# Kernel tuning notes

Measured on AMD Instinct MI355X. Metric: run time of the kernel, lower is better.

The kernel has to match this reference:

```python
import jax, jax.numpy as jnp
import numpy as np

N = 50000      # nodes
E = 800000     # edges (avg degree 16)
F_IN = 64      # node_features (== GENConv out, so no input projection)
H = 64         # hidden
EXP = 2 * H    # GENConv MLP expansion dim = 128
D2 = F_IN + H  # dense-block concat dim = SAGEConv in = 128
EPS_MSG = 1e-7 # GENConv message eps
BN_EPS = 1e-5


def setup_inputs() -> dict:
    key = jax.random.key(0)
    ks = jax.random.split(key, 16)
    g = lambda k, shape, fan: jax.random.normal(k, shape, jnp.float32) / np.sqrt(fan)
    return {
        "x": jax.random.normal(ks[0], (N, F_IN), jnp.float32),
        "edge_index": jax.random.randint(ks[1], (2, E), 0, N, jnp.int32),
        # GENConv MLP: Linear(64,128) -> BatchNorm(128) -> ReLU -> Linear(128,64)
        "W1": g(ks[2], (H, EXP), H), "b1": jnp.zeros((EXP,), jnp.float32),
        "gamma": jnp.ones((EXP,), jnp.float32), "beta": jnp.zeros((EXP,), jnp.float32),
        "W2": g(ks[3], (EXP, H), EXP), "b2": jnp.zeros((H,), jnp.float32),
        # SAGEConv project Linear(128,128), lin_l Linear(128,64), lin_r Linear(128,64,bias=False)
        "Wp": g(ks[4], (D2, D2), D2), "bp": jnp.zeros((D2,), jnp.float32),
        "Wl": g(ks[5], (D2, H), D2), "bl": jnp.zeros((H,), jnp.float32),
        "Wr": g(ks[6], (D2, H), D2),
        # fc Linear(64,1)
        "Wf": g(ks[7], (H, 1), H), "bf": jnp.zeros((1,), jnp.float32),
    }


def _forward(x, W1, b1, gamma, beta, W2, b2, Wp, bp, Wl, bl, Wr, Wf, bf, src, dst):
    n = x.shape[0]
    # ---- GENConv(aggr='softmax', t=1.0): msg = relu(x_j) + eps -------------
    msg = jax.nn.relu(x[src]) + EPS_MSG                       # [E, H]
    mmax = jax.ops.segment_max(msg, dst, num_segments=n)      # per-dst, per-feature max
    mmax = jax.lax.stop_gradient(jnp.where(jnp.isfinite(mmax), mmax, 0.0))
    e = jnp.exp(msg - mmax[dst])                              # t = 1.0
    denom = jax.ops.segment_sum(e, dst, num_segments=n)
    numer = jax.ops.segment_sum(e * msg, dst, num_segments=n)
    agg = numer / jnp.where(denom > 0, denom, 1.0)            # softmax aggregation
    out = agg + x                                             # residual with x_dst
    # GENConv MLP (BatchNorm in training mode: batch stats, biased var)
    h = out @ W1 + b1
    mu = h.mean(axis=0)
    var = h.var(axis=0)
    h = (h - mu) * jax.lax.rsqrt(var + BN_EPS) * gamma + beta
    h = jax.nn.relu(h) @ W2 + b2                              # [N, H]
    # ---- DeepGCNLayer block='dense': concat input ---------------------------
    x2 = jnp.concatenate([x, h], axis=-1)                     # [N, F_IN+H]
    x2 = jax.nn.sigmoid(x2)                                   # self.relu = Sigmoid()
    # ---- SAGEConv(project=True, aggr=DeepSetsAggregation()==sum) -----------
    xp = jax.nn.relu(x2 @ Wp + bp)                            # projected source feats
    aggr = jax.ops.segment_sum(xp[src], dst, num_segments=n)  # DeepSets w/o nns = sum
    out2 = aggr @ Wl + bl + x2 @ Wr                           # root uses UNprojected x2
    out2 = jax.nn.sigmoid(out2)
    logits = out2 @ Wf + bf                                   # [N, 1]
    probs = jax.nn.sigmoid(logits)                            # training branch
    return probs, logits


def reference(x, edge_index, W1, b1, gamma, beta, W2, b2, Wp, bp, Wl, bl, Wr, Wf, bf):
    src, dst = edge_index[0], edge_index[1]
    return _forward(x, W1, b1, gamma, beta, W2, b2, Wp, bp, Wl, bl, Wr, Wf, bf, src, dst)
```

## Files before the change

### kernel.cpp

```cpp
#include <hip/hip_runtime.h>

#define F_IN 64
#define HID 64
#define EXPD 128
#define D2 128
#define MAXDEG 64
#define NBW 128
#define NB 391
#define NBINB 98
#define SUBCAP 64
#define EPT 32

typedef __attribute__((ext_vector_type(8))) short bf16x8;
typedef __attribute__((ext_vector_type(4))) float f32x4;

__device__ __forceinline__ float sigmoidf_(float x) {
    return 1.0f / (1.0f + __expf(-x));
}
__device__ __forceinline__ unsigned bf16rne_(float f) {
    unsigned u = __float_as_uint(f);
    return (u + 0x7FFFu + ((u >> 16) & 1u)) >> 16;
}
__device__ __forceinline__ float bf16tof_(unsigned u16) {
    return __uint_as_float(u16 << 16);
}

__global__ __launch_bounds__(256) void k_bin(const int* __restrict__ ei,
                                             int* __restrict__ cnt2,
                                             unsigned* __restrict__ binned2,
                                             const float* __restrict__ x,
                                             unsigned short* __restrict__ x16,
                                             const float* __restrict__ W1,
                                             const float* __restrict__ W2,
                                             const float* __restrict__ Wp,
                                             const float* __restrict__ Wl,
                                             const float* __restrict__ Wr,
                                             short* __restrict__ dst,
                                             float* __restrict__ bnsums,
                                             int nE, int n, int nbinb) {
    int b = blockIdx.x;
    int tid = threadIdx.x;
    if (b < nbinb) {
        __shared__ int hist[NB];
        if (b == 0) bnsums[tid] = 0.f;
        for (int i = tid; i < NB; i += 256) hist[i] = 0;
        __syncthreads();
        unsigned ed[EPT];
        unsigned short rk[EPT];
        int e0 = b * (256 * EPT);
#pragma unroll
        for (int j = 0; j < EPT; ++j) {
            int e = e0 + j * 256 + tid;
            if (e < nE) {
                unsigned s = (unsigned)ei[e];
                unsigned d = (unsigned)ei[nE + e];
                ed[j] = s | (d << 16);
                rk[j] = (unsigned short)atomicAdd(&hist[d >> 7], 1);
            }
        }
        __syncthreads();
        for (int i = tid; i < NB; i += 256) cnt2[b * NB + i] = hist[i];
#pragma unroll
        for (int j = 0; j < EPT; ++j) {
            int e = e0 + j * 256 + tid;
            if (e < nE) {
                int bin = (ed[j] >> 16) >> 7;
                int r = (int)rk[j];
                if (r < SUBCAP)
                    binned2[((size_t)bin * nbinb + b) * SUBCAP + r] = ed[j];
            }
        }
        return;
    }
    b -= nbinb;
    if (b < 192) {
        int e = b * 256 + tid;
        const float* src;
        int K, N, base2;
        if (e < 8192)       { src = W1; K = 64;  N = 128; base2 = 0; }
        else if (e < 16384) { src = W2; K = 128; N = 64;  base2 = 8192; }
        else if (e < 32768) { src = Wp; K = 128; N = 128; base2 = 16384; }
        else if (e < 40960) { src = Wl; K = 128; N = 64;  base2 = 32768; }
        else                { src = Wr; K = 128; N = 64;  base2 = 40960; }
        int le = e - base2;
        int j = le & 7;
        int lane = (le >> 3) & 63;
        int n16 = lane & 15, q = lane >> 4;
        int rest = le >> 9;
        int KC = K / 32;
        int kc = rest % KC, nt = rest / KC;
        int k = kc * 32 + q * 8 + j;
        int col = nt * 16 + n16;
        dst[e] = (short)bf16rne_(src[(size_t)k * N + col]);
        return;
    }
    int i0 = (b - 192) * 1024 + tid * 4;
    if (i0 < n * F_IN) {
        float4 v = *(const float4*)(x + i0);
        uint2 pk;
        pk.x = bf16rne_(v.x) | (bf16rne_(v.y) << 16);
        pk.y = bf16rne_(v.z) | (bf16rne_(v.w) << 16);
        *(uint2*)(x16 + i0) = pk;
    }
}

__global__ __launch_bounds__(256) void k_csr(const int* __restrict__ cnt2,
                                             const unsigned* __restrict__ binned2,
                                             int* __restrict__ counts,
                                             unsigned short* __restrict__ csr,
                                             int n, int nbinb) {
    __shared__ unsigned short lcsr[NBW * MAXDEG];
    __shared__ int lcnt[NBW];
    __shared__ int scnt[NBINB];
    int b = blockIdx.x;
    int tid = threadIdx.x;
    if (tid < NBW) lcnt[tid] = 0;
    for (int i = tid; i < nbinb; i += 256) {
        int c = cnt2[i * NB + b];
        scnt[i] = c < SUBCAP ? c : SUBCAP;
    }
    __syncthreads();
    const unsigned* src = binned2 + (size_t)b * nbinb * SUBCAP;
    int tot = nbinb * SUBCAP;
    for (int i = tid; i < tot; i += 256) {
        int blk = i >> 6;
        int r = i & (SUBCAP - 1);
        if (r < scnt[blk]) {
            unsigned u = src[i];
            int dl = (int)(u >> 16) - b * NBW;
            int slot = atomicAdd(&lcnt[dl], 1);
            if (slot < MAXDEG) lcsr[dl * MAXDEG + slot] = (unsigned short)(u & 0xFFFF);
        }
    }
    __syncthreads();
    int nodebase = b * NBW;
    if (tid < NBW && nodebase + tid < n) counts[nodebase + tid] = lcnt[tid];
    int nrows = n - nodebase;
    nrows = nrows < NBW ? nrows : NBW;
    int nu4 = nrows * 8;
    uint4* dstrow = (uint4*)(csr + (size_t)nodebase * MAXDEG);
    for (int idx = tid; idx < nu4; idx += 256) dstrow[idx] = ((const uint4*)lcsr)[idx];
}

__global__ __launch_bounds__(1024) void k_geng(const unsigned short* __restrict__ x16,
                                               const int* __restrict__ counts,
                                               const unsigned short* __restrict__ csr,
                                               const short* __restrict__ Wf,
                                               const float* __restrict__ b1,
                                               unsigned short* __restrict__ h16,
                                               float* __restrict__ bnsums, int n) {
    __shared__ short As[64 * 64];
    __shared__ float bnred[256];
    const unsigned* x32 = (const unsigned*)x16;
    int tid = threadIdx.x;
    int w = tid >> 6;
    int lane = tid & 63;
    int H = lane >> 5, f2 = lane & 31;
    int rblk = blockIdx.x * 64;
    if (tid < 256) bnred[tid] = 0.f;
    for (int t = 0; t < 4; ++t) {
        int rr = w * 4 + t;
        int v = rblk + rr;
        int q8 = f2 >> 2;
        int slot = ((rr >> 4) * 2 + (q8 >> 2)) * 64 + (q8 & 3) * 16 + (rr & 15);
        if (v < n) {
            int deg = counts[v];
            deg = deg > MAXDEG ? MAXDEG : deg;
            int idx = 0;
            if (lane < deg) idx = (int)csr[(size_t)v * MAXDEG + lane];
            float d0 = 0.f, d1 = 0.f, n0 = 0.f, n1 = 0.f;
            int i = 0;
            for (; i + 8 <= deg; i += 8) {
                int sA = __shfl(idx, i + 0 + H, 64);
                int sB = __shfl(idx, i + 2 + H, 64);
                int sC = __shfl(idx, i + 4 + H, 64);
                int sD = __shfl(idx, i + 6 + H, 64);
                unsigned uA = x32[(size_t)sA * 32 + f2];
                unsigned uB = x32[(size_t)sB * 32 + f2];
                unsigned uC = x32[(size_t)sC * 32 + f2];
                unsigned uD = x32[(size_t)sD * 32 + f2];
#pragma unroll
                for (int tt = 0; tt < 4; ++tt) {
                    unsigned u = tt == 0 ? uA : tt == 1 ? uB : tt == 2 ? uC : uD;
                    float m0 = fmaxf(bf16tof_(u & 0xFFFF), 0.f) + 1e-7f;
                    float m1 = fmaxf(bf16tof_(u >> 16), 0.f) + 1e-7f;
                    float e0 = __expf(m0), e1 = __expf(m1);
                    d0 += e0; d1 += e1;
                    n0 = fmaf(e0, m0, n0);
                    n1 = fmaf(e1, m1, n1);
                }
            }
            for (; i + 2 <= deg; i += 2) {
                int s = __shfl(idx, i + H, 64);
                unsigned u = x32[(size_t)s * 32 + f2];
                float m0 = fmaxf(bf16tof_(u & 0xFFFF), 0.f) + 1e-7f;
                float m1 = fmaxf(bf16tof_(u >> 16), 0.f) + 1e-7f;
                float e0 = __expf(m0), e1 = __expf(m1);
                d0 += e0; d1 += e1;
                n0 = fmaf(e0, m0, n0);
                n1 = fmaf(e1, m1, n1);
            }
            if (i < deg) {
                int s = __shfl(idx, i, 64);
                if (H == 0) {
                    unsigned u = x32[(size_t)s * 32 + f2];
                    float m0 = fmaxf(bf16tof_(u & 0xFFFF), 0.f) + 1e-7f;
                    float m1 = fmaxf(bf16tof_(u >> 16), 0.f) + 1e-7f;
                    float e0 = __expf(m0), e1 = __expf(m1);
                    d0 += e0; d1 += e1;
                    n0 = fmaf(e0, m0, n0);
                    n1 = fmaf(e1, m1, n1);
                }
            }
            d0 += __shfl_xor(d0, 32, 64);
            d1 += __shfl_xor(d1, 32, 64);
            n0 += __shfl_xor(n0, 32, 64);
            n1 += __shfl_xor(n1, 32, 64);
            if (H == 0) {
                float a0 = (deg > 0) ? (n0 / d0) : 0.f;
                float a1 = (deg > 0) ? (n1 / d1) : 0.f;
                unsigned xv = x32[(size_t)v * 32 + f2];
                float r0 = a0 + bf16tof_(xv & 0xFFFF);
                float r1 = a1 + bf16tof_(xv >> 16);
                *(unsigned*)(As + slot * 8 + (f2 & 3) * 2) =
                    bf16rne_(r0) | (bf16rne_(r1) << 16);
            }
        } else {
            if (H == 0) *(unsigned*)(As + slot * 8 + (f2 & 3) * 2) = 0u;
        }
    }
    __syncthreads();
    int L = lane;
    int q = L >> 4, n16 = L & 15;
    int mt = w & 3;
    int nt_base = (w >> 2) * 2;
    f32x4 acc[2];
#pragma unroll
    for (int nt = 0; nt < 2; ++nt) acc[nt] = (f32x4){0.f, 0.f, 0.f, 0.f};
#pragma unroll
    for (int kc = 0; kc < 2; ++kc) {
        bf16x8 a = *(const bf16x8*)(As + ((mt * 2 + kc) * 64 + L) * 8);
#pragma unroll
        for (int nt = 0; nt < 2; ++nt) {
            bf16x8 b = *(const bf16x8*)(Wf + (size_t)(((nt_base + nt) * 2 + kc) * 64 + L) * 8);
            acc[nt] = __builtin_amdgcn_mfma_f32_16x16x32_bf16(a, b, acc[nt], 0, 0, 0);
        }
    }
#pragma unroll
    for (int nt = 0; nt < 2; ++nt) {
        int col = (nt_base + nt) * 16 + n16;
        float bv = b1[col];
        float s = 0.f, s2 = 0.f;
#pragma unroll
        for (int r = 0; r < 4; ++r) {
            int row = rblk + mt * 16 + q * 4 + r;
            float hv = acc[nt][r] + bv;
            if (row < n) {
                h16[(size_t)row * EXPD + col] = (unsigned short)bf16rne_(hv);
                s += hv;
                s2 = fmaf(hv, hv, s2);
            }
        }
        s += __shfl_xor(s, 16, 64);
        s += __shfl_xor(s, 32, 64);
        s2 += __shfl_xor(s2, 16, 64);
        s2 += __shfl_xor(s2, 32, 64);
        if (q == 0) {
            atomicAdd(&bnred[col], s);
            atomicAdd(&bnred[128 + col], s2);
        }
    }
    __syncthreads();
    if (tid < 256) atomicAdd(&bnsums[tid], bnred[tid]);
}

__global__ __launch_bounds__(256) void k_mlp2ab(const unsigned short* __restrict__ h16,
                                                const float* __restrict__ bnsums,
                                                const float* __restrict__ gamma,
                                                const float* __restrict__ beta,
                                                const short* __restrict__ Wf2,
                                                const float* __restrict__ b2,
                                                const unsigned short* __restrict__ x16,
                                                const short* __restrict__ Wfp,
                                                const short* __restrict__ Wfl,
                                                const short* __restrict__ Wfr,
                                                const float* __restrict__ bp,
                                                unsigned short* __restrict__ yp16,
                                                unsigned short* __restrict__ yr16,
                                                float inv_n, int n) {
    __shared__ short Bs[64 * 128];
    __shared__ short As[64 * 128];
    __shared__ float ssl[256];
    int tid = threadIdx.x;
    int rblk = blockIdx.x * 64;
    if (tid < 128) {
        float mu = bnsums[tid] * inv_n;
        float var = fmaf(-mu, mu, bnsums[128 + tid] * inv_n);
        float rs = rsqrtf(fmaxf(var, 0.f) + 1e-5f);
        float scale = gamma[tid] * rs;
        ssl[tid] = scale;
        ssl[128 + tid] = fmaf(-mu, scale, beta[tid]);
    }
    __syncthreads();
#pragma unroll
    for (int it = 0; it < 4; ++it) {
        int c = it * 256 + tid;
        int rr = c & 63, q8 = c >> 6;
        int gr = rblk + rr;
        gr = gr < n ? gr : n - 1;
        uint4 v = *(const uint4*)(h16 + (size_t)gr * EXPD + q8 * 8);
        float4 sc1 = *(const float4*)(ssl + q8 * 8);
        float4 sc2 = *(const float4*)(ssl + q8 * 8 + 4);
        float4 sh1 = *(const float4*)(ssl + 128 + q8 * 8);
        float4 sh2 = *(const float4*)(ssl + 128 + q8 * 8 + 4);
        float o0 = fmaxf(fmaf(bf16tof_(v.x & 0xFFFF), sc1.x, sh1.x), 0.f);
        float o1 = fmaxf(fmaf(bf16tof_(v.x >> 16),    sc1.y, sh1.y), 0.f);
        float o2 = fmaxf(fmaf(bf16tof_(v.y & 0xFFFF), sc1.z, sh1.z), 0.f);
        float o3 = fmaxf(fmaf(bf16tof_(v.y >> 16),    sc1.w, sh1.w), 0.f);
        float o4 = fmaxf(fmaf(bf16tof_(v.z & 0xFFFF), sc2.x, sh2.x), 0.f);
        float o5 = fmaxf(fmaf(bf16tof_(v.z >> 16),    sc2.y, sh2.y), 0.f);
        float o6 = fmaxf(fmaf(bf16tof_(v.w & 0xFFFF), sc2.z, sh2.z), 0.f);
        float o7 = fmaxf(fmaf(bf16tof_(v.w >> 16),    sc2.w, sh2.w), 0.f);
        uint4 pk;
        pk.x = bf16rne_(o0) | (bf16rne_(o1) << 16);
        pk.y = bf16rne_(o2) | (bf16rne_(o3) << 16);
        pk.z = bf16rne_(o4) | (bf16rne_(o5) << 16);
        pk.w = bf16rne_(o6) | (bf16rne_(o7) << 16);
        int slot = ((rr >> 4) * 4 + (q8 >> 2)) * 64 + (q8 & 3) * 16 + (rr & 15);
        *(uint4*)(Bs + slot * 8) = pk;
    }
#pragma unroll
    for (int it = 0; it < 2; ++it) {
        int c = it * 256 + tid;
        int rr = c & 63, q8 = c >> 6;
        int gr = rblk + rr;
        gr = gr < n ? gr : n - 1;
        uint4 v = *(const uint4*)(x16 + (size_t)gr * F_IN + q8 * 8);
        float o0 = sigmoidf_(bf16tof_(v.x & 0xFFFF));
        float o1 = sigmoidf_(bf16tof_(v.x >> 16));
        float o2 = sigmoidf_(bf16tof_(v.y & 0xFFFF));
        float o3 = sigmoidf_(bf16tof_(v.y >> 16));
        float o4 = sigmoidf_(bf16tof_(v.z & 0xFFFF));
        float o5 = sigmoidf_(bf16tof_(v.z >> 16));
        float o6 = sigmoidf_(bf16tof_(v.w & 0xFFFF));
        float o7 = sigmoidf_(bf16tof_(v.w >> 16));
        uint4 pk;
        pk.x = bf16rne_(o0) | (bf16rne_(o1) << 16);
        pk.y = bf16rne_(o2) | (bf16rne_(o3) << 16);
        pk.z = bf16rne_(o4) | (bf16rne_(o5) << 16);
        pk.w = bf16rne_(o6) | (bf16rne_(o7) << 16);
        int slot = ((rr >> 4) * 4 + (q8 >> 2)) * 64 + (q8 & 3) * 16 + (rr & 15);
        *(uint4*)(As + slot * 8) = pk;
    }
    __syncthreads();
    int L = tid & 63, w = tid >> 6;
    int q = L >> 4, n16 = L & 15;
    {
        int mtb = (w & 1) * 2, ntb = (w >> 1) * 2;
        f32x4 acch[2][2];
#pragma unroll
        for (int mt = 0; mt < 2; ++mt)
#pragma unroll
            for (int nt = 0; nt < 2; ++nt) acch[mt][nt] = (f32x4){0.f, 0.f, 0.f, 0.f};
#pragma unroll
        for (int kc = 0; kc < 4; ++kc) {
            bf16x8 a0 = *(const bf16x8*)(Bs + (((mtb + 0) * 4 + kc) * 64 + L) * 8);
            bf16x8 a1 = *(const bf16x8*)(Bs + (((mtb + 1) * 4 + kc) * 64 + L) * 8);
#pragma unroll
            for (int nt = 0; nt < 2; ++nt) {
                bf16x8 b = *(const bf16x8*)(Wf2 + (size_t)(((ntb + nt) * 4 + kc) * 64 + L) * 8);
                acch[0][nt] = __builtin_amdgcn_mfma_f32_16x16x32_bf16(a0, b, acch[0][nt], 0, 0, 0);
                acch[1][nt] = __builtin_amdgcn_mfma_f32_16x16x32_bf16(a1, b, acch[1][nt], 0, 0, 0);
            }
        }
#pragma unroll
        for (int nt = 0; nt < 2; ++nt) {
            int col = (ntb + nt) * 16 + n16;
            float bv = b2[col];
            int q8b = 8 + (col >> 3), jb = col & 7;
#pragma unroll
            for (int mt = 0; mt < 2; ++mt)
#pragma unroll
                for (int r = 0; r < 4; ++r) {
                    int rr2 = (w & 1) * 32 + mt * 16 + q * 4 + r;
                    float hv = sigmoidf_(acch[mt][nt][r] + bv);
                    int slot = ((rr2 >> 4) * 4 + (q8b >> 2)) * 64 + (q8b & 3) * 16 + (rr2 & 15);
                    As[slot * 8 + jb] = (short)bf16rne_(hv);
                }
        }
    }
    __syncthreads();
    int mt_base = (w & 1) * 2;
    int nt_base = (w >> 1) * 4;
    f32x4 acc[2][4];
    f32x4 accr[2][2];
#pragma unroll
    for (int mt = 0; mt < 2; ++mt) {
#pragma unroll
        for (int nt = 0; nt < 4; ++nt) acc[mt][nt] = (f32x4){0.f, 0.f, 0.f, 0.f};
#pragma unroll
        for (int nt = 0; nt < 2; ++nt) accr[mt][nt] = (f32x4){0.f, 0.f, 0.f, 0.f};
    }
#pragma unroll
    for (int kc = 0; kc < 4; ++kc) {
        bf16x8 a0 = *(const bf16x8*)(As + (((mt_base + 0) * 4 + kc) * 64 + L) * 8);
        bf16x8 a1 = *(const bf16x8*)(As + (((mt_base + 1) * 4 + kc) * 64 + L) * 8);
#pragma unroll
        for (int nt = 0; nt < 4; ++nt) {
            bf16x8 b = *(const bf16x8*)(Wfp + (size_t)(((nt_base + nt) * 4 + kc) * 64 + L) * 8);
            acc[0][nt] = __builtin_amdgcn_mfma_f32_16x16x32_bf16(a0, b, acc[0][nt], 0, 0, 0);
            acc[1][nt] = __builtin_amdgcn_mfma_f32_16x16x32_bf16(a1, b, acc[1][nt], 0, 0, 0);
        }
#pragma unroll
        for (int nt = 0; nt < 2; ++nt) {
            bf16x8 b = *(const bf16x8*)(Wfr + (size_t)((((w >> 1) * 2 + nt) * 4 + kc) * 64 + L) * 8);
            accr[0][nt] = __builtin_amdgcn_mfma_f32_16x16x32_bf16(a0, b, accr[0][nt], 0, 0, 0);
            accr[1][nt] = __builtin_amdgcn_mfma_f32_16x16x32_bf16(a1, b, accr[1][nt], 0, 0, 0);
        }
    }
#pragma unroll
    for (int nt = 0; nt < 2; ++nt) {
        int col = ((w >> 1) * 2 + nt) * 16 + n16;
#pragma unroll
        for (int mt = 0; mt < 2; ++mt)
#pragma unroll
            for (int r = 0; r < 4; ++r) {
                int row = rblk + (w & 1) * 32 + mt * 16 + q * 4 + r;
                if (row < n)
                    yr16[(size_t)row * HID + col] = (unsigned short)bf16rne_(accr[mt][nt][r]);
            }
    }
#pragma unroll
    for (int nt = 0; nt < 4; ++nt) {
        int kk = (nt_base + nt) * 16 + n16;
        float bv = bp[kk];
        int q8b = kk >> 3, jb = kk & 7;
#pragma unroll
        for (int mt = 0; mt < 2; ++mt)
#pragma unroll
            for (int r = 0; r < 4; ++r) {
                int rr2 = (w & 1) * 32 + mt * 16 + q * 4 + r;
                float xv = fmaxf(acc[mt][nt][r] + bv, 0.f);
                int slot = ((rr2 >> 4) * 4 + (q8b >> 2)) * 64 + (q8b & 3) * 16 + (rr2 & 15);
                Bs[slot * 8 + jb] = (short)bf16rne_(xv);
            }
    }
    __syncthreads();
    f32x4 acc2[4];
#pragma unroll
    for (int nt = 0; nt < 4; ++nt) acc2[nt] = (f32x4){0.f, 0.f, 0.f, 0.f};
#pragma unroll
    for (int kc = 0; kc < 4; ++kc) {
        bf16x8 a = *(const bf16x8*)(Bs + ((w * 4 + kc) * 64 + L) * 8);
#pragma unroll
        for (int nt = 0; nt < 4; ++nt) {
            bf16x8 b = *(const bf16x8*)(Wfl + (size_t)((nt * 4 + kc) * 64 + L) * 8);
            acc2[nt] = __builtin_amdgcn_mfma_f32_16x16x32_bf16(a, b, acc2[nt], 0, 0, 0);
        }
    }
#pragma unroll
    for (int nt = 0; nt < 4; ++nt) {
        int col = nt * 16 + n16;
#pragma unroll
        for (int r = 0; r < 4; ++r) {
            int row = rblk + w * 16 + q * 4 + r;
            if (row < n)
                yp16[(size_t)row * HID + col] = (unsigned short)bf16rne_(acc2[nt][r]);
        }
    }
}

__global__ __launch_bounds__(256) void k_sagef(const unsigned short* __restrict__ yp16,
                                               const int* __restrict__ counts,
                                               const unsigned short* __restrict__ csr,
                                               const unsigned short* __restrict__ yr16,
                                               const float* __restrict__ bl,
                                               const float* __restrict__ Wfv,
                                               const float* __restrict__ bf,
                                               float* __restrict__ out, int n) {
    const unsigned* yp32 = (const unsigned*)yp16;
    int wid = threadIdx.x >> 6;
    int lane = threadIdx.x & 63;
    int H = lane >> 5, f2 = lane & 31;
    int v = blockIdx.x * 4 + wid;
    if (v >= n) return;
    int deg = counts[v];
    deg = deg > MAXDEG ? MAXDEG : deg;
    int idx = 0;
    if (lane < deg) idx = (int)csr[(size_t)v * MAXDEG + lane];
    float a0 = 0.f, a1 = 0.f;
    int i = 0;
    for (; i + 8 <= deg; i += 8) {
        int sA = __shfl(idx, i + 0 + H, 64);
        int sB = __shfl(idx, i + 2 + H, 64);
        int sC = __shfl(idx, i + 4 + H, 64);
        int sD = __shfl(idx, i + 6 + H, 64);
        unsigned uA = yp32[(size_t)sA * 32 + f2];
        unsigned uB = yp32[(size_t)sB * 32 + f2];
        unsigned uC = yp32[(size_t)sC * 32 + f2];
        unsigned uD = yp32[(size_t)sD * 32 + f2];
        a0 += bf16tof_(uA & 0xFFFF) + bf16tof_(uB & 0xFFFF) +
              bf16tof_(uC & 0xFFFF) + bf16tof_(uD & 0xFFFF);
        a1 += bf16tof_(uA >> 16) + bf16tof_(uB >> 16) +
              bf16tof_(uC >> 16) + bf16tof_(uD >> 16);
    }
    for (; i + 2 <= deg; i += 2) {
        int s = __shfl(idx, i + H, 64);
        unsigned u = yp32[(size_t)s * 32 + f2];
        a0 += bf16tof_(u & 0xFFFF);
        a1 += bf16tof_(u >> 16);
    }
    if (i < deg) {
        int s = __shfl(idx, i, 64);
        if (H == 0) {
            unsigned u = yp32[(size_t)s * 32 + f2];
            a0 += bf16tof_(u & 0xFFFF);
            a1 += bf16tof_(u >> 16);
        }
    }
    a0 += __shfl_xor(a0, 32, 64);
    a1 += __shfl_xor(a1, 32, 64);
    if (H == 0) {
        unsigned u = ((const unsigned*)yr16)[(size_t)v * 32 + f2];
        float2 blv = ((const float2*)bl)[f2];
        float2 wv  = ((const float2*)Wfv)[f2];
        float o0 = sigmoidf_(a0 + blv.x + bf16tof_(u & 0xFFFF));
        float o1 = sigmoidf_(a1 + blv.y + bf16tof_(u >> 16));
        float t = fmaf(o0, wv.x, o1 * wv.y);
        t += __shfl_xor(t, 1, 64);
        t += __shfl_xor(t, 2, 64);
        t += __shfl_xor(t, 4, 64);
        t += __shfl_xor(t, 8, 64);
        t += __shfl_xor(t, 16, 64);
        if (f2 == 0) {
            float lg = t + bf[0];
            out[v] = sigmoidf_(lg);
            out[n + v] = lg;
        }
    }
}

extern "C" void kernel_launch(void* const* d_in, const int* in_sizes, int n_in,
                              void* d_out, int out_size, void* d_ws, size_t ws_size,
                              hipStream_t stream) {
    const float* x     = (const float*)d_in[0];
    const int*   ei    = (const int*)d_in[1];
    const float* W1    = (const float*)d_in[2];
    const float* b1    = (const float*)d_in[3];
    const float* gamma = (const float*)d_in[4];
    const float* beta  = (const float*)d_in[5];
    const float* W2    = (const float*)d_in[6];
    const float* b2    = (const float*)d_in[7];
    const float* Wp    = (const float*)d_in[8];
    const float* bp    = (const float*)d_in[9];
    const float* Wl    = (const float*)d_in[10];
    const float* bl    = (const float*)d_in[11];
    const float* Wr    = (const float*)d_in[12];
    const float* Wfv   = (const float*)d_in[13];
    const float* bf    = (const float*)d_in[14];
    const int n = in_sizes[0] / F_IN;
    const int e = in_sizes[1] / 2;

    char* ws = (char*)d_ws;
    size_t off = 0;
    auto alloc = [&](size_t bytes) -> void* {
        void* p = (void*)(ws + off);
        off += (bytes + 255) & ~(size_t)255;
        return p;
    };
    const int nbinb = (e + 256 * EPT - 1) / (256 * EPT);
    float*          bnsums   = (float*)alloc(256 * 4);
    int*            cnt2     = (int*)alloc((size_t)nbinb * NB * 4);
    int*            counts   = (int*)alloc((size_t)n * 4);
    unsigned short* csr      = (unsigned short*)alloc((size_t)n * MAXDEG * 2);
    unsigned*       binned2  = (unsigned*)alloc((size_t)NB * nbinb * SUBCAP * 4);
    unsigned short* x16      = (unsigned short*)alloc((size_t)n * F_IN * 2);
    unsigned short* h16      = (unsigned short*)alloc((size_t)n * EXPD * 2);
    unsigned short* yp16     = (unsigned short*)alloc((size_t)n * HID * 2);
    unsigned short* yr16     = (unsigned short*)alloc((size_t)n * HID * 2);
    short*          wfrag    = (short*)alloc(49152 * 2);

    float* out = (float*)d_out;
    const int nb64  = (n + 63) / 64;
    const int nb4   = (n + 3) / 4;
    const int nfp = nbinb + 192 + ((n * F_IN + 1023) / 1024);

    k_bin<<<nfp, 256, 0, stream>>>(ei, cnt2, binned2, x, x16, W1, W2, Wp, Wl,
                                   Wr, wfrag, bnsums, e, n, nbinb);
    k_csr<<<NB, 256, 0, stream>>>(cnt2, binned2, counts, csr, n, nbinb);
    k_geng<<<nb64, 1024, 0, stream>>>(x16, counts, csr, wfrag, b1, h16, bnsums, n);
    k_mlp2ab<<<nb64, 256, 0, stream>>>(h16, bnsums, gamma, beta, wfrag + 8192, b2,
                                       x16, wfrag + 16384, wfrag + 32768,
                                       wfrag + 40960, bp, yp16, yr16,
                                       1.0f / (float)n, n);
    k_sagef<<<nb4, 256, 0, stream>>>(yp16, counts, csr, yr16, bl, Wfv, bf, out, n);
}
```

Baseline: 210.1 us.

## Restructure GENConv gather to 4 edges per wave with 8-byte loads and smaller blocks

The softmax-aggregation gather in k_geng now splits each wave into four 16-lane groups, each handling one edge per step with 8-byte (4 bf16) loads, instead of two 32-lane halves doing 4-byte loads. The next row is loaded before the current one is processed to hide latency. The block shrinks from 1024 threads and 64 rows to 512 threads and 32 rows, with the MFMA tile mapping adjusted to match. This costs an extra cross-lane reduction step, and the 32-row blocks must still line up with the epilogue tiling, which is not shown.

```diff
diff --git a/kernel.cpp b/kernel.cpp
--- a/kernel.cpp
+++ b/kernel.cpp
@@ -23,6 +23,18 @@
 }
 __device__ __forceinline__ float bf16tof_(unsigned u16) {
     return __uint_as_float(u16 << 16);
+}
+__device__ __forceinline__ void gen_acc4_(uint2 u, float& d0, float& d1, float& d2,
+                                          float& d3, float& n0, float& n1, float& n2,
+                                          float& n3) {
+    float m0 = fmaxf(bf16tof_(u.x & 0xFFFF), 0.f) + 1e-7f;
+    float m1 = fmaxf(bf16tof_(u.x >> 16), 0.f) + 1e-7f;
+    float m2 = fmaxf(bf16tof_(u.y & 0xFFFF), 0.f) + 1e-7f;
+    float m3 = fmaxf(bf16tof_(u.y >> 16), 0.f) + 1e-7f;
+    float e0 = __expf(m0), e1 = __expf(m1), e2 = __expf(m2), e3 = __expf(m3);
+    d0 += e0; d1 += e1; d2 += e2; d3 += e3;
+    n0 = fmaf(e0, m0, n0); n1 = fmaf(e1, m1, n1);
+    n2 = fmaf(e2, m2, n2); n3 = fmaf(e3, m3, n3);
 }
 
 __global__ __launch_bounds__(256) void k_bin(const int* __restrict__ ei,
@@ -142,98 +154,99 @@
     for (int idx = tid; idx < nu4; idx += 256) dstrow[idx] = ((const uint4*)lcsr)[idx];
 }
 
-__global__ __launch_bounds__(1024) void k_geng(const unsigned short* __restrict__ x16,
-                                               const int* __restrict__ counts,
-                                               const unsigned short* __restrict__ csr,
-                                               const short* __restrict__ Wf,
-                                               const float* __restrict__ b1,
-                                               unsigned short* __restrict__ h16,
-                                               float* __restrict__ bnsums, int n) {
-    __shared__ short As[64 * 64];
+__global__ __launch_bounds__(512) void k_geng(const unsigned short* __restrict__ x16,
+                                              const int* __restrict__ counts,
+                                              const unsigned short* __restrict__ csr,
+                                              const short* __restrict__ Wf,
+                                              const float* __restrict__ b1,
+                                              unsigned short* __restrict__ h16,
+                                              float* __restrict__ bnsums, int n) {
+    __shared__ short As[32 * 64];
     __shared__ float bnred[256];
-    const unsigned* x32 = (const unsigned*)x16;
+    const uint2* x64 = (const uint2*)x16;
     int tid = threadIdx.x;
     int w = tid >> 6;
     int lane = tid & 63;
-    int H = lane >> 5, f2 = lane & 31;
-    int rblk = blockIdx.x * 64;
+    int grp = lane >> 4;
+    int fl = lane & 15;
+    int rblk = blockIdx.x * 32;
     if (tid < 256) bnred[tid] = 0.f;
     for (int t = 0; t < 4; ++t) {
         int rr = w * 4 + t;
         int v = rblk + rr;
-        int q8 = f2 >> 2;
+        int q8 = fl >> 1, j0 = (fl & 1) * 4;
         int slot = ((rr >> 4) * 2 + (q8 >> 2)) * 64 + (q8 & 3) * 16 + (rr & 15);
         if (v < n) {
             int deg = counts[v];
             deg = deg > MAXDEG ? MAXDEG : deg;
             int idx = 0;
             if (lane < deg) idx = (int)csr[(size_t)v * MAXDEG + lane];
-            float d0 = 0.f, d1 = 0.f, n0 = 0.f, n1 = 0.f;
-            int i = 0;
-            for (; i + 8 <= deg; i += 8) {
-                int sA = __shfl(idx, i + 0 + H, 64);
-                int sB = __shfl(idx, i + 2 + H, 64);
-                int sC = __shfl(idx, i + 4 + H, 64);
-                int sD = __shfl(idx, i + 6 + H, 64);
-                unsigned uA = x32[(size_t)sA * 32 + f2];
-                unsigned uB = x32[(size_t)sB * 32 + f2];
-                unsigned uC = x32[(size_t)sC * 32 + f2];
-                unsigned uD = x32[(size_t)sD * 32 + f2];
-#pragma unroll
-                for (int tt = 0; tt < 4; ++tt) {
-                    unsigned u = tt == 0 ? uA : tt == 1 ? uB : tt == 2 ? uC : uD;
-                    float m0 = fmaxf(bf16tof_(u & 0xFFFF), 0.f) + 1e-7f;
-                    float m1 = fmaxf(bf16tof_(u >> 16), 0.f) + 1e-7f;
-                    float e0 = __expf(m0), e1 = __expf(m1);
-                    d0 += e0; d1 += e1;
-                    n0 = fmaf(e0, m0, n0);
-                    n1 = fmaf(e1, m1, n1);
+            float d0 = 0.f, d1 = 0.f, d2 = 0.f, d3 = 0.f;
+            float n0 = 0.f, n1 = 0.f, n2 = 0.f, n3 = 0.f;
+            int deg4 = deg & ~3;
+            if (deg4 > 0) {
+                int s = __shfl(idx, grp, 64);
+                uint2 u = x64[(size_t)s * 16 + fl];
+                for (int i = 4; i < deg4; i += 4) {
+                    int s2 = __shfl(idx, i + grp, 64);
+                    uint2 u2 = x64[(size_t)s2 * 16 + fl];
+                    gen_acc4_(u, d0, d1, d2, d3, n0, n1, n2, n3);
+                    u = u2;
                 }
-            }
-            for (; i + 2 <= deg; i += 2) {
-                int s = __shfl(idx, i + H, 64);
-                unsigned u = x32[(size_t)s * 32 + f2];
-                float m0 = fmaxf(bf16tof_(u & 0xFFFF), 0.f) + 1e-7f;
-                float m1 = fmaxf(bf16tof_(u >> 16), 0.f) + 1e-7f;
-                float e0 = __expf(m0), e1 = __expf(m1);
-                d0 += e0; d1 += e1;
-                n0 = fmaf(e0, m0, n0);
-                n1 = fmaf(e1, m1, n1);
-            }
-            if (i < deg) {
-                int s = __shfl(idx, i, 64);
-                if (H == 0) {
-                    unsigned u = x32[(size_t)s * 32 + f2];
-                    float m0 = fmaxf(bf16tof_(u & 0xFFFF), 0.f) + 1e-7f;
-                    float m1 = fmaxf(bf16tof_(u >> 16), 0.f) + 1e-7f;
-                    float e0 = __expf(m0), e1 = __expf(m1);
-                    d0 += e0; d1 += e1;
-                    n0 = fmaf(e0, m0, n0);
-                    n1 = fmaf(e1, m1, n1);
-                }
-            }
-            d0 += __shfl_xor(d0, 32, 64);
-            d1 += __shfl_xor(d1, 32, 64);
-            n0 += __shfl_xor(n0, 32, 64);
-            n1 += __shfl_xor(n1, 32, 64);
-            if (H == 0) {
+                gen_acc4_(u, d0, d1, d2, d3, n0, n1, n2, n3);
+            }
+            if (deg > deg4) {
+                int ii = deg4 + grp;
+                int s = __shfl(idx, ii, 64);
+                uint2 u = x64[(size_t)s * 16 + fl];
+                bool act = ii < deg;
+                float m0 = fmaxf(bf16tof_(u.x & 0xFFFF), 0.f) + 1e-7f;
+                float m1 = fmaxf(bf16tof_(u.x >> 16), 0.f) + 1e-7f;
+                float m2 = fmaxf(bf16tof_(u.y & 0xFFFF), 0.f) + 1e-7f;
+                float m3 = fmaxf(bf16tof_(u.y >> 16), 0.f) + 1e-7f;
+                float e0 = act ? __expf(m0) : 0.f;
+                float e1 = act ? __expf(m1) : 0.f;
+                float e2 = act ? __expf(m2) : 0.f;
+                float e3 = act ? __expf(m3) : 0.f;
+                d0 += e0; d1 += e1; d2 += e2; d3 += e3;
+                n0 = fmaf(e0, m0, n0); n1 = fmaf(e1, m1, n1);
+                n2 = fmaf(e2, m2, n2); n3 = fmaf(e3, m3, n3);
+            }
+            d0 += __shfl_xor(d0, 16, 64); d0 += __shfl_xor(d0, 32, 64);
+            d1 += __shfl_xor(d1, 16, 64); d1 += __shfl_xor(d1, 32, 64);
+            d2 += __shfl_xor(d2, 16, 64); d2 += __shfl_xor(d2, 32, 64);
+            d3 += __shfl_xor(d3, 16, 64); d3 += __shfl_xor(d3, 32, 64);
+            n0 += __shfl_xor(n0, 16, 64); n0 += __shfl_xor(n0, 32, 64);
+            n1 += __shfl_xor(n1, 16, 64); n1 += __shfl_xor(n1, 32, 64);
+            n2 += __shfl_xor(n2, 16, 64); n2 += __shfl_xor(n2, 32, 64);
+            n3 += __shfl_xor(n3, 16, 64); n3 += __shfl_xor(n3, 32, 64);
+            if (grp == 0) {
                 float a0 = (deg > 0) ? (n0 / d0) : 0.f;
                 float a1 = (deg > 0) ? (n1 / d1) : 0.f;
-                unsigned xv = x32[(size_t)v * 32 + f2];
-                float r0 = a0 + bf16tof_(xv & 0xFFFF);
-                float r1 = a1 + bf16tof_(xv >> 16);
-                *(unsigned*)(As + slot * 8 + (f2 & 3) * 2) =
-                    bf16rne_(r0) | (bf16rne_(r1) << 16);
+                float a2 = (deg > 0) ? (n2 / d2) : 0.f;
+                float a3 = (deg > 0) ? (n3 / d3) : 0.f;
+                uint2 xv = x64[(size_t)v * 16 + fl];
+                float r0 = a0 + bf16tof_(xv.x & 0xFFFF);
+                float r1 = a1 + bf16tof_(xv.x >> 16);
+                float r2 = a2 + bf16tof_(xv.y & 0xFFFF);
+                float r3 = a3 + bf16tof_(xv.y >> 16);
+                uint2 pk;
+                pk.x = bf16rne_(r0) | (bf16rne_(r1) << 16);
+                pk.y = bf16rne_(r2) | (bf16rne_(r3) << 16);
+                *(uint2*)(As + slot * 8 + j0) = pk;
             }
         } else {
-            if (H == 0) *(unsigned*)(As + slot * 8 + (f2 & 3) * 2) = 0u;
+            if (grp == 0) {
+                uint2 z; z.x = 0u; z.y = 0u;
+                *(uint2*)(As + slot * 8 + j0) = z;
+            }
         }
     }
     __syncthreads();
     int L = lane;
     int q = L >> 4, n16 = L & 15;
-    int mt = w & 3;
-    int nt_base = (w >> 2) * 2;
+    int mt = w & 1;
+    int nt_base = (w >> 1) * 2;
     f32x4 acc[2];
 #pragma unroll
     for (int nt = 0; nt < 2; ++nt) acc[nt] = (f32x4){0.f, 0.f, 0.f, 0.f};
@@ -582,13 +595,14 @@
 
     float* out = (float*)d_out;
     const int nb64  = (n + 63) / 64;
+    const int nb32  = (n + 31) / 32;
     const int nb4   = (n + 3) / 4;
     const int nfp = nbinb + 192 + ((n * F_IN + 1023) / 1024);
 
     k_bin<<<nfp, 256, 0, stream>>>(ei, cnt2, binned2, x, x16, W1, W2, Wp, Wl,
                                    Wr, wfrag, bnsums, e, n, nbinb);
     k_csr<<<NB, 256, 0, stream>>>(cnt2, binned2, counts, csr, n, nbinb);
-    k_geng<<<nb64, 1024, 0, stream>>>(x16, counts, csr, wfrag, b1, h16, bnsums, n);
+    k_geng<<<nb32, 512, 0, stream>>>(x16, counts, csr, wfrag, b1, h16, bnsums, n);
     k_mlp2ab<<<nb64, 256, 0, stream>>>(h16, bnsums, gamma, beta, wfrag + 8192, b2,
                                        x16, wfrag + 16384, wfrag + 32768,
                                        wfrag + 40960, bp, yp16, yr16,
```

Result: slower. 222.5 us (+5.9%).

## Precompute per-node exp and exp*msg pairs, gather them in GENConv aggregation

Applied to the files above, without the earlier changes.

Because the softmax shift is dropped, each edge's contribution depends only on its source node, so exp(m) and exp(m)*m are now computed once per node feature in the conversion kernel and stored as fp32 pairs. The aggregation kernel then only gathers and sums these pairs, with no per-edge exp. Each lane handles one feature over a whole row, and the block shrinks to 32 rows with 512 threads. The cost is that the gathered data grows from 2-byte bf16 to 8-byte float2 per feature, quadrupling gather traffic per edge. In exchange the values are computed from full-precision x rather than the bf16 copy.

```diff
diff --git a/kernel.cpp b/kernel.cpp
--- a/kernel.cpp
+++ b/kernel.cpp
@@ -30,6 +30,7 @@
                                              unsigned* __restrict__ binned2,
                                              const float* __restrict__ x,
                                              unsigned short* __restrict__ x16,
+                                             float* __restrict__ Ef,
                                              const float* __restrict__ W1,
                                              const float* __restrict__ W2,
                                              const float* __restrict__ Wp,
@@ -101,6 +102,15 @@
         pk.x = bf16rne_(v.x) | (bf16rne_(v.y) << 16);
         pk.y = bf16rne_(v.z) | (bf16rne_(v.w) << 16);
         *(uint2*)(x16 + i0) = pk;
+        float m0 = fmaxf(v.x, 0.f) + 1e-7f;
+        float m1 = fmaxf(v.y, 0.f) + 1e-7f;
+        float m2 = fmaxf(v.z, 0.f) + 1e-7f;
+        float m3 = fmaxf(v.w, 0.f) + 1e-7f;
+        float e0 = __expf(m0), e1 = __expf(m1), e2 = __expf(m2), e3 = __expf(m3);
+        float4 pa = {e0, e0 * m0, e1, e1 * m1};
+        float4 pb = {e2, e2 * m2, e3, e3 * m3};
+        *(float4*)(Ef + (size_t)i0 * 2) = pa;
+        *(float4*)(Ef + (size_t)i0 * 2 + 4) = pb;
     }
 }
 
@@ -142,98 +152,75 @@
     for (int idx = tid; idx < nu4; idx += 256) dstrow[idx] = ((const uint4*)lcsr)[idx];
 }
 
-__global__ __launch_bounds__(1024) void k_geng(const unsigned short* __restrict__ x16,
-                                               const int* __restrict__ counts,
-                                               const unsigned short* __restrict__ csr,
-                                               const short* __restrict__ Wf,
-                                               const float* __restrict__ b1,
-                                               unsigned short* __restrict__ h16,
-                                               float* __restrict__ bnsums, int n) {
-    __shared__ short As[64 * 64];
+__global__ __launch_bounds__(512) void k_geng(const float* __restrict__ x,
+                                              const float* __restrict__ Ef,
+                                              const int* __restrict__ counts,
+                                              const unsigned short* __restrict__ csr,
+                                              const short* __restrict__ Wf,
+                                              const float* __restrict__ b1,
+                                              unsigned short* __restrict__ h16,
+                                              float* __restrict__ bnsums, int n) {
+    __shared__ short As[32 * 64];
     __shared__ float bnred[256];
-    const unsigned* x32 = (const unsigned*)x16;
     int tid = threadIdx.x;
     int w = tid >> 6;
     int lane = tid & 63;
-    int H = lane >> 5, f2 = lane & 31;
-    int rblk = blockIdx.x * 64;
+    int rblk = blockIdx.x * 32;
     if (tid < 256) bnred[tid] = 0.f;
+    int q8 = lane >> 3, jb = lane & 7;
     for (int t = 0; t < 4; ++t) {
         int rr = w * 4 + t;
         int v = rblk + rr;
-        int q8 = f2 >> 2;
         int slot = ((rr >> 4) * 2 + (q8 >> 2)) * 64 + (q8 & 3) * 16 + (rr & 15);
+        float hval = 0.f;
         if (v < n) {
             int deg = counts[v];
             deg = deg > MAXDEG ? MAXDEG : deg;
             int idx = 0;
             if (lane < deg) idx = (int)csr[(size_t)v * MAXDEG + lane];
-            float d0 = 0.f, d1 = 0.f, n0 = 0.f, n1 = 0.f;
+            float den = 0.f, num = 0.f;
             int i = 0;
             for (; i + 8 <= deg; i += 8) {
-                int sA = __shfl(idx, i + 0 + H, 64);
-                int sB = __shfl(idx, i + 2 + H, 64);
-                int sC = __shfl(idx, i + 4 + H, 64);
-                int sD = __shfl(idx, i + 6 + H, 64);
-                unsigned uA = x32[(size_t)sA * 32 + f2];
-                unsigned uB = x32[(size_t)sB * 32 + f2];
-                unsigned uC = x32[(size_t)sC * 32 + f2];
-                unsigned uD = x32[(size_t)sD * 32 + f2];
-#pragma unroll
-                for (int tt = 0; tt < 4; ++tt) {
-                    unsigned u = tt == 0 ? uA : tt == 1 ? uB : tt == 2 ? uC : uD;
-                    float m0 = fmaxf(bf16tof_(u & 0xFFFF), 0.f) + 1e-7f;
-                    float m1 = fmaxf(bf16tof_(u >> 16), 0.f) + 1e-7f;
-                    float e0 = __expf(m0), e1 = __expf(m1);
-                    d0 += e0; d1 += e1;
-                    n0 = fmaf(e0, m0, n0);
-                    n1 = fmaf(e1, m1, n1);
-                }
-            }
-            for (; i + 2 <= deg; i += 2) {
-                int s = __shfl(idx, i + H, 64);
-                unsigned u = x32[(size_t)s * 32 + f2];
-                float m0 = fmaxf(bf16tof_(u & 0xFFFF), 0.f) + 1e-7f;
-                float m1 = fmaxf(bf16tof_(u >> 16), 0.f) + 1e-7f;
-                float e0 = __expf(m0), e1 = __expf(m1);
-                d0 += e0; d1 += e1;
-                n0 = fmaf(e0, m0, n0);
-                n1 = fmaf(e1, m1, n1);
-            }
-            if (i < deg) {
+                int s0 = __shfl(idx, i + 0, 64);
+                int s1 = __shfl(idx, i + 1, 64);
+                int s2 = __shfl(idx, i + 2, 64);
+                int s3 = __shfl(idx, i + 3, 64);
+                int s4 = __shfl(idx, i + 4, 64);
+                int s5 = __shfl(idx, i + 5, 64);
+                int s6 = __shfl(idx, i + 6, 64);
+                int s7 = __shfl(idx, i + 7, 64);
+                float2 u0 = *(const float2*)(Ef + ((unsigned)s0 << 7) + lane * 2);
+                float2 u1 = *(const float2*)(Ef + ((unsigned)s1 << 7) + lane * 2);
+                float2 u2 = *(const float2*)(Ef + ((unsigned)s2 << 7) + lane * 2);
+                float2 u3 = *(const float2*)(Ef + ((unsigned)s3 << 7) + lane * 2);
+                float2 u4 = *(const float2*)(Ef + ((unsigned)s4 << 7) + lane * 2);
+                float2 u5 = *(const float2*)(Ef + ((unsigned)s5 << 7) + lane * 2);
+                float2 u6 = *(const float2*)(Ef + ((unsigned)s6 << 7) + lane * 2);
+                float2 u7 = *(const float2*)(Ef + ((unsigned)s7 << 7) + lane * 2);
+                den += u0.x; num += u0.y;
+                den += u1.x; num += u1.y;
+                den += u2.x; num += u2.y;
+                den += u3.x; num += u3.y;
+                den += u4.x; num += u4.y;
+                den += u5.x; num += u5.y;
+                den += u6.x; num += u6.y;
+                den += u7.x; num += u7.y;
+            }
+            for (; i < deg; ++i) {
                 int s = __shfl(idx, i, 64);
-                if (H == 0) {
-                    unsigned u = x32[(size_t)s * 32 + f2];
-                    float m0 = fmaxf(bf16tof_(u & 0xFFFF), 0.f) + 1e-7f;
-                    float m1 = fmaxf(bf16tof_(u >> 16), 0.f) + 1e-7f;
-                    float e0 = __expf(m0), e1 = __expf(m1);
-                    d0 += e0; d1 += e1;
-                    n0 = fmaf(e0, m0, n0);
-                    n1 = fmaf(e1, m1, n1);
-                }
-            }
-            d0 += __shfl_xor(d0, 32, 64);
-            d1 += __shfl_xor(d1, 32, 64);
-            n0 += __shfl_xor(n0, 32, 64);
-            n1 += __shfl_xor(n1, 32, 64);
-            if (H == 0) {
-                float a0 = (deg > 0) ? (n0 / d0) : 0.f;
-                float a1 = (deg > 0) ? (n1 / d1) : 0.f;
-                unsigned xv = x32[(size_t)v * 32 + f2];
-                float r0 = a0 + bf16tof_(xv & 0xFFFF);
-                float r1 = a1 + bf16tof_(xv >> 16);
-                *(unsigned*)(As + slot * 8 + (f2 & 3) * 2) =
-                    bf16rne_(r0) | (bf16rne_(r1) << 16);
-            }
-        } else {
-            if (H == 0) *(unsigned*)(As + slot * 8 + (f2 & 3) * 2) = 0u;
-        }
+                float2 u = *(const float2*)(Ef + ((unsigned)s << 7) + lane * 2);
+                den += u.x; num += u.y;
+            }
+            float a = (deg > 0) ? (num / den) : 0.f;
+            hval = a + x[(size_t)v * F_IN + lane];
+        }
+        As[slot * 8 + jb] = (short)bf16rne_(hval);
     }
     __syncthreads();
     int L = lane;
     int q = L >> 4, n16 = L & 15;
-    int mt = w & 3;
-    int nt_base = (w >> 2) * 2;
+    int mt = w & 1;
+    int nt_base = (w >> 1) * 2;
     f32x4 acc[2];
 #pragma unroll
     for (int nt = 0; nt < 2; ++nt) acc[nt] = (f32x4){0.f, 0.f, 0.f, 0.f};
@@ -575,6 +562,7 @@
     unsigned short* csr      = (unsigned short*)alloc((size_t)n * MAXDEG * 2);
     unsigned*       binned2  = (unsigned*)alloc((size_t)NB * nbinb * SUBCAP * 4);
     unsigned short* x16      = (unsigned short*)alloc((size_t)n * F_IN * 2);
+    float*          Ef       = (float*)alloc((size_t)n * F_IN * 8);
     unsigned short* h16      = (unsigned short*)alloc((size_t)n * EXPD * 2);
     unsigned short* yp16     = (unsigned short*)alloc((size_t)n * HID * 2);
     unsigned short* yr16     = (unsigned short*)alloc((size_t)n * HID * 2);
@@ -582,13 +570,14 @@
 
     float* out = (float*)d_out;
     const int nb64  = (n + 63) / 64;
+    const int nb32  = (n + 31) / 32;
     const int nb4   = (n + 3) / 4;
     const int nfp = nbinb + 192 + ((n * F_IN + 1023) / 1024);
 
-    k_bin<<<nfp, 256, 0, stream>>>(ei, cnt2, binned2, x, x16, W1, W2, Wp, Wl,
+    k_bin<<<nfp, 256, 0, stream>>>(ei, cnt2, binned2, x, x16, Ef, W1, W2, Wp, Wl,
                                    Wr, wfrag, bnsums, e, n, nbinb);
     k_csr<<<NB, 256, 0, stream>>>(cnt2, binned2, counts, csr, n, nbinb);
-    k_geng<<<nb64, 1024, 0, stream>>>(x16, counts, csr, wfrag, b1, h16, bnsums, n);
+    k_geng<<<nb32, 512, 0, stream>>>(x, Ef, counts, csr, wfrag, b1, h16, bnsums, n);
     k_mlp2ab<<<nb64, 256, 0, stream>>>(h16, bnsums, gamma, beta, wfrag + 8192, b2,
                                        x16, wfrag + 16384, wfrag + 32768,
                                        wfrag + 40960, bp, yp16, yr16,
```

New measurement: 245.0 us. 16.6% more time.
